# Optimization experiments

Measured on AMD Instinct MI355X. Metric: run time of the kernel, lower is better.

The kernel has to match this reference:

```python
import jax, jax.numpy as jnp
import numpy as np

HID = 4096; H = 32; KVH = 8; D = 128
B = 4; Q = 256; KV = 2048; HIST = KV - Q
BS = 64; NB = KV // BS; NBLOCKS = 160
WINDOW = 1024; THETA = 10000.0


def _rope(x, pos):
    # x: [T, heads, D], pos: [T] absolute positions
    half = D // 2
    inv = 1.0 / (THETA ** (jnp.arange(half, dtype=jnp.float32) / half))
    f = pos.astype(jnp.float32)[:, None] * inv[None, :]          # [T, D/2]
    cos = jnp.concatenate([jnp.cos(f), jnp.cos(f)], -1)[:, None, :]
    sin = jnp.concatenate([jnp.sin(f), jnp.sin(f)], -1)[:, None, :]
    x1, x2 = jnp.split(x, 2, axis=-1)
    return x * cos + jnp.concatenate([-x2, x1], -1) * sin


def setup_inputs() -> dict:
    key = jax.random.key(0)
    ks = jax.random.split(key, 7)
    T = B * Q
    return dict(
        hidden_states=jax.random.normal(ks[0], (T, HID), jnp.float32),
        wq=jax.random.normal(ks[1], (HID, H * D), jnp.float32) * 0.02,
        wk=jax.random.normal(ks[2], (HID, KVH * D), jnp.float32) * 0.02,
        wv=jax.random.normal(ks[3], (HID, KVH * D), jnp.float32) * 0.02,
        wo=jax.random.normal(ks[4], (H * D, HID), jnp.float32) * 0.02,
        k_cache=jax.random.normal(ks[5], (NBLOCKS, BS, KVH, D), jnp.float32),
        v_cache=jax.random.normal(ks[6], (NBLOCKS, BS, KVH, D), jnp.float32),
        # each sequence appends Q new tokens at positions [HIST, KV)
        position_ids=jnp.tile(HIST + jnp.arange(Q, dtype=jnp.int32), B),
        q_start_loc=jnp.arange(B, dtype=jnp.int32) * Q,
        q_seq_length=jnp.full((B,), Q, jnp.int32),
        kv_seq_length=jnp.full((B,), KV, jnp.int32),
        block_offsets=jnp.arange(B * NB, dtype=jnp.int32).reshape(B, NB),
    )


def reference(hidden_states, wq, wk, wv, wo, k_cache, v_cache,
              position_ids, q_start_loc, q_seq_length, kv_seq_length,
              block_offsets):
    # qkv proj (no bias, Mistral)
    q = (hidden_states @ wq).reshape(-1, H, D)    # [T, H, D]
    k = (hidden_states @ wk).reshape(-1, KVH, D)  # [T, KVH, D]
    v = (hidden_states @ wv).reshape(-1, KVH, D)
    # rotary embedding on q, k with per-token absolute positions
    q = _rope(q, position_ids)
    k = _rope(k, position_ids)
    # fill paged KV cache: token with in-sequence slot s of sequence b goes to
    # block block_offsets[b, s // BS], offset s % BS
    b_idx = jnp.repeat(jnp.arange(B), Q)
    blk = block_offsets[b_idx, position_ids // BS]
    off = position_ids % BS
    k_cache = k_cache.at[blk, off].set(k)
    v_cache = v_cache.at[blk, off].set(v)
    # paged attention: gather each sequence's blocks from the cache
    k_all = k_cache[block_offsets].reshape(B, KV, KVH, D)
    v_all = v_cache[block_offsets].reshape(B, KV, KVH, D)
    G = H // KVH  # GQA group size
    qb = q.reshape(B, Q, KVH, G, D)
    scores = jnp.einsum('bqhgd,bkhd->bhgqk', qb, k_all) / jnp.sqrt(jnp.float32(D))
    # causal + sliding-window mask on absolute positions
    qpos = HIST + jnp.arange(Q)
    kpos = jnp.arange(KV)
    valid = (kpos[None, :] <= qpos[:, None]) & (kpos[None, :] > qpos[:, None] - WINDOW)
    scores = jnp.where(valid[None, None, None], scores, -jnp.inf)
    p = jax.nn.softmax(scores, axis=-1)
    o = jnp.einsum('bhgqk,bkhd->bqhgd', p, v_all).reshape(B * Q, H * D)
    return o @ wo
```

## Files before the change

### kernel.cpp

```cpp
#include <hip/hip_runtime.h>

#define BSZ  4
#define QL   256
#define KVL  2048
#define HIST 1792
#define WIN  1024
#define NH   32
#define NKVH 8
#define DH   128
#define HID  4096
#define SCALE 0.088388347648318447f
#define MFIX  8.0f

typedef __bf16 bf16x8 __attribute__((ext_vector_type(8)));
typedef float  fx4    __attribute__((ext_vector_type(4)));
typedef unsigned short us4 __attribute__((ext_vector_type(4)));
typedef unsigned short us8 __attribute__((ext_vector_type(8)));

__device__ __forceinline__ unsigned short f2bf(float x) {
    unsigned u = __float_as_uint(x);
    u += 0x7FFFu + ((u >> 16) & 1u);
    return (unsigned short)(u >> 16);
}
__device__ __forceinline__ float bf2f(unsigned short h) {
    return __uint_as_float(((unsigned)h) << 16);
}
__device__ __forceinline__ fx4 mfma16(bf16x8 a, bf16x8 b, fx4 c) {
    return __builtin_amdgcn_mfma_f32_16x16x32_bf16(a, b, c, 0, 0, 0);
}
__device__ __forceinline__ bf16x8 ldb16(const unsigned short* p) {
    return *reinterpret_cast<const bf16x8*>(p);
}

typedef __attribute__((address_space(1))) const void gv_t;
typedef __attribute__((address_space(3))) void lv_t;
__device__ __forceinline__ void gl16(const void* g, void* l) {
    __builtin_amdgcn_global_load_lds((gv_t*)g, (lv_t*)l, 16, 0, 0);
}

__device__ __forceinline__ void gemm_body(
    const unsigned short* __restrict__ A, const unsigned short* __restrict__ B,
    float* __restrict__ C0, float* __restrict__ Cz, size_t czstride,
    int lda, int ldb, int ldc, int ksteps, int klast, int nx, int ny, int nz)
{
    constexpr int TILE = 128 * 32;
    __shared__ __align__(16) unsigned short lds[3 * 2 * TILE];

    const int per = gridDim.x >> 3;
    const int t = (blockIdx.x & 7) * per + (blockIdx.x >> 3);
    const int bx = t % nx;
    const int by = (t / nx) % ny;
    const int bz = t / (nx * ny);

    const int row0 = bx * 128;
    const int col0 = by * 128;
    const int kbase = bz * ksteps * 32;
    const int nks = (bz == nz - 1) ? klast : ksteps;
    float* Cm = (bz == 0) ? C0 : (Cz + (size_t)(bz - 1) * czstride);

    const int tid  = threadIdx.x;
    const int lane = tid & 63;
    const int w    = tid >> 6;
    const int wr   = w >> 1, wc = w & 1;
    const int l16  = lane & 15;
    const int lg   = lane >> 4;
    const int r_in = lane >> 2;
    const int c8   = (lane & 3) * 8;

    fx4 acc[4][4] = {};

    auto STAGE = [&](int bufi, int kp) {
        unsigned short* Lb = lds + bufi * (2 * TILE);
#pragma unroll
        for (int i = 0; i < 2; ++i) {
            const int r = w * 32 + i * 16 + r_in;
            const int ldsb = (w * 2 + i) * 512;
            gl16(A + (size_t)(row0 + r) * lda + kp + c8, Lb + ldsb);
            gl16(B + (size_t)(col0 + r) * ldb + kp + c8, Lb + TILE + ldsb);
        }
    };

    STAGE(0, kbase);
    STAGE(1, kbase + 32);
    for (int ks = 0; ks < nks; ++ks) {
        if (ks + 2 < nks) {
            STAGE((ks + 2) % 3, kbase + (ks + 2) * 32);
            asm volatile("s_waitcnt vmcnt(8)" ::: "memory");
        } else if (ks + 1 < nks) {
            asm volatile("s_waitcnt vmcnt(4)" ::: "memory");
        } else {
            asm volatile("s_waitcnt vmcnt(0)" ::: "memory");
        }
        __builtin_amdgcn_s_barrier();
        __builtin_amdgcn_sched_barrier(0);

        const unsigned short* Lb = lds + (ks % 3) * (2 * TILE);
        const unsigned short* AhT = Lb;
        const unsigned short* BhT = Lb + TILE;

        bf16x8 af[4], bfv[4];
#pragma unroll
        for (int f = 0; f < 4; ++f) {
            af[f]  = ldb16(AhT + (wr * 64 + f * 16 + l16) * 32 + lg * 8);
            bfv[f] = ldb16(BhT + (wc * 64 + f * 16 + l16) * 32 + lg * 8);
        }
        __builtin_amdgcn_s_setprio(1);
#pragma unroll
        for (int fr = 0; fr < 4; ++fr)
#pragma unroll
            for (int fc = 0; fc < 4; ++fc)
                acc[fr][fc] = mfma16(af[fr], bfv[fc], acc[fr][fc]);
        __builtin_amdgcn_s_setprio(0);
        __builtin_amdgcn_sched_barrier(0);
        __builtin_amdgcn_s_barrier();
    }
#pragma unroll
    for (int fr = 0; fr < 4; ++fr)
#pragma unroll
        for (int fc = 0; fc < 4; ++fc) {
            const size_t rbase = (size_t)(row0 + wr * 64 + fr * 16 + lg * 4);
            const int col = col0 + wc * 64 + fc * 16 + l16;
#pragma unroll
            for (int r = 0; r < 4; ++r)
                Cm[(rbase + r) * ldc + col] = acc[fr][fc][r];
        }
}

__global__ __launch_bounds__(256) void qkv_gemm_kernel(
    const unsigned short* __restrict__ A, const unsigned short* __restrict__ B,
    float* __restrict__ C0, float* __restrict__ Cz, size_t czstride,
    int lda, int ldb, int ldc, int ksteps, int klast, int nx, int ny, int nz)
{
    gemm_body(A, B, C0, Cz, czstride, lda, ldb, ldc, ksteps, klast, nx, ny, nz);
}

__global__ __launch_bounds__(256) void oproj_gemm_kernel(
    const unsigned short* __restrict__ A, const unsigned short* __restrict__ B,
    float* __restrict__ C0, float* __restrict__ Cz, size_t czstride,
    int lda, int ldb, int ldc, int ksteps, int klast, int nx, int ny, int nz)
{
    gemm_body(A, B, C0, Cz, czstride, lda, ldb, ldc, ksteps, klast, nx, ny, nz);
}

__device__ __forceinline__ void transpose_tile(
    const float* __restrict__ w, unsigned short* __restrict__ hi, int N,
    int n0, int k0)
{
    __shared__ unsigned short sh[64][72];
    const int tid = threadIdx.x;
    const int rr = tid >> 4;
    const int cc = (tid & 15) * 4;
#pragma unroll
    for (int p = 0; p < 4; ++p) {
        const int kl = p * 16 + rr;
        fx4 v = *reinterpret_cast<const fx4*>(w + (size_t)(k0 + kl) * N + n0 + cc);
#pragma unroll
        for (int j = 0; j < 4; ++j)
            sh[cc + j][kl] = f2bf(v[j]);
    }
    __syncthreads();
    const int nl = tid >> 2;
    const int kc = (tid & 3) * 16;
    unsigned short* oh = hi + (size_t)(n0 + nl) * 4096 + k0 + kc;
    *reinterpret_cast<us8*>(oh)     = *reinterpret_cast<const us8*>(&sh[nl][kc]);
    *reinterpret_cast<us8*>(oh + 8) = *reinterpret_cast<const us8*>(&sh[nl][kc + 8]);
}

__global__ __launch_bounds__(256) void prep_kernel(
    const float* __restrict__ wq, const float* __restrict__ wk,
    const float* __restrict__ wv, const float* __restrict__ wo,
    const float* __restrict__ hs,
    unsigned short* __restrict__ wqkvT, unsigned short* __restrict__ woTh,
    unsigned short* __restrict__ hsb, float* __restrict__ tab)
{
    const int r = blockIdx.x;
    const int tid = threadIdx.x;
    if (r < 4096) {
        transpose_tile(wq, wqkvT, 4096, (r & 63) * 64, (r >> 6) * 64);
    } else if (r < 5120) {
        const int r2 = r - 4096;
        transpose_tile(wk, wqkvT + (size_t)4096 * 4096, 1024,
                       (r2 & 15) * 64, (r2 >> 4) * 64);
    } else if (r < 6144) {
        const int r2 = r - 5120;
        transpose_tile(wv, wqkvT + (size_t)5120 * 4096, 1024,
                       (r2 & 15) * 64, (r2 >> 4) * 64);
    } else if (r < 10240) {
        const int r2 = r - 6144;
        transpose_tile(wo, woTh, 4096, (r2 & 63) * 64, (r2 >> 6) * 64);
    } else if (r < 12288) {
        const int r2 = r - 10240;
        int i = r2 * 256 + tid;
#pragma unroll
        for (int rep = 0; rep < 2; ++rep) {
            fx4 v = reinterpret_cast<const fx4*>(hs)[i];
            us4 o;
#pragma unroll
            for (int j = 0; j < 4; ++j) o[j] = f2bf(v[j]);
            reinterpret_cast<us4*>(hsb)[i] = o;
            i += 524288;
        }
    } else {
        const int r2 = r - 12288;
        const int qi = r2 * 4 + (tid >> 6);
        const int jr = tid & 63;
        const float inv = powf(10000.f, -(float)jr * (1.f / 64.f));
        const float f = (float)(HIST + qi) * inv;
        float s, c;
        sincosf(f, &s, &c);
        tab[(qi * 64 + jr) * 2]     = c;
        tab[(qi * 64 + jr) * 2 + 1] = s;
    }
}

__global__ __launch_bounds__(256) void rope_q_kernel(
    const float* __restrict__ qkv0, const float* __restrict__ qkv1,
    const int* __restrict__ pos_ids, const float* __restrict__ tab,
    unsigned short* __restrict__ qb)
{
    const int t = blockIdx.x;
    const int b = t >> 8;
    const int qi = t & 255;
    const int pi = pos_ids[t] - HIST;
    const int tid = threadIdx.x;
    const int h = tid >> 3;
    const int d0 = (tid & 7) * 8;
    const float* q0 = qkv0 + (size_t)t * 6144 + h * DH;
    const float* q1 = qkv1 + (size_t)t * 6144 + h * DH;
    float xl[8], xh[8];
    *reinterpret_cast<fx4*>(&xl[0]) = *reinterpret_cast<const fx4*>(q0 + d0)
                                    + *reinterpret_cast<const fx4*>(q1 + d0);
    *reinterpret_cast<fx4*>(&xl[4]) = *reinterpret_cast<const fx4*>(q0 + d0 + 4)
                                    + *reinterpret_cast<const fx4*>(q1 + d0 + 4);
    *reinterpret_cast<fx4*>(&xh[0]) = *reinterpret_cast<const fx4*>(q0 + d0 + 64)
                                    + *reinterpret_cast<const fx4*>(q1 + d0 + 64);
    *reinterpret_cast<fx4*>(&xh[4]) = *reinterpret_cast<const fx4*>(q0 + d0 + 68)
                                    + *reinterpret_cast<const fx4*>(q1 + d0 + 68);
    us8 outl, outh;
#pragma unroll
    for (int i = 0; i < 8; ++i) {
        const int jr = d0 + i;
        const float c = tab[(pi * 64 + jr) * 2];
        const float s = tab[(pi * 64 + jr) * 2 + 1];
        outl[i] = f2bf(xl[i] * c - xh[i] * s);
        outh[i] = f2bf(xh[i] * c + xl[i] * s);
    }
    unsigned short* dst = qb + (((size_t)b * NH + h) * QL + qi) * DH;
    *reinterpret_cast<us8*>(dst + d0)      = outl;
    *reinterpret_cast<us8*>(dst + d0 + 64) = outh;
}

__global__ __launch_bounds__(256) void gather_kv_kernel(
    const float* __restrict__ qkv0, const float* __restrict__ qkv1,
    const float* __restrict__ k_cache, const float* __restrict__ v_cache,
    const int* __restrict__ block_offsets, const float* __restrict__ tab,
    unsigned short* __restrict__ k_all, unsigned short* __restrict__ vT)
{
    __shared__ unsigned short vls[32][136];
    const int bid = blockIdx.x;
    const int xcd = bid & 7;
    const int i = bid >> 3;
    const int g = ((i & 31) << 3) | xcd;
    const int kh = i >> 5;
    const int b  = g >> 6;
    const int ck = g & 63;
    const int kv0 = ck * 32;
    const int tid = threadIdx.x;
    const int tok = tid >> 3;
    const int sl  = tid & 7;
    const int kvpos = kv0 + tok;
    const bool is_old = (kvpos < HIST);

    float x[16];
    float v[16];
    if (is_old) {
        const int blk = block_offsets[b * 32 + (kvpos >> 6)];
        const size_t base = (((size_t)blk * 64 + (kvpos & 63)) * NKVH + kh) * DH + sl * 4;
        const float* sk = k_cache + base;
        const float* sv = v_cache + base;
#pragma unroll
        for (int j = 0; j < 4; ++j) {
            *reinterpret_cast<fx4*>(&x[j * 4]) = *reinterpret_cast<const fx4*>(sk + j * 32);
            *reinterpret_cast<fx4*>(&v[j * 4]) = *reinterpret_cast<const fx4*>(sv + j * 32);
        }
    } else {
        const int t = b * QL + (kvpos - HIST);
        const int pi = kvpos - HIST;
        const size_t tb = (size_t)t * 6144 + kh * DH + sl * 4;
        const float* k0p = qkv0 + tb + 4096;
        const float* k1p = qkv1 + tb + 4096;
        const float* v0p = qkv0 + tb + 5120;
        const float* v1p = qkv1 + tb + 5120;
#pragma unroll
        for (int j = 0; j < 4; ++j) {
            *reinterpret_cast<fx4*>(&x[j * 4]) =
                *reinterpret_cast<const fx4*>(k0p + j * 32) +
                *reinterpret_cast<const fx4*>(k1p + j * 32);
            *reinterpret_cast<fx4*>(&v[j * 4]) =
                *reinterpret_cast<const fx4*>(v0p + j * 32) +
                *reinterpret_cast<const fx4*>(v1p + j * 32);
        }
#pragma unroll
        for (int j = 0; j < 2; ++j) {
            const int jr0 = sl * 4 + j * 32;
            fx4 cs0 = *reinterpret_cast<const fx4*>(tab + ((size_t)pi * 64 + jr0) * 2);
            fx4 cs1 = *reinterpret_cast<const fx4*>(tab + ((size_t)pi * 64 + jr0) * 2 + 4);
            const float c[4] = {cs0[0], cs0[2], cs1[0], cs1[2]};
            const float s[4] = {cs0[1], cs0[3], cs1[1], cs1[3]};
#pragma unroll
            for (int e = 0; e < 4; ++e) {
                const float lo = x[j * 4 + e], hi = x[(j + 2) * 4 + e];
                x[j * 4 + e]       = lo * c[e] - hi * s[e];
                x[(j + 2) * 4 + e] = hi * c[e] + lo * s[e];
            }
        }
    }
    {
        const size_t tbase = (((size_t)b * NKVH + kh) * KVL + kv0) * DH;
#pragma unroll
        for (int j = 0; j < 4; ++j) {
            const int d = sl * 4 + j * 32;
            const int dc = d >> 3;
            us4 pk;
#pragma unroll
            for (int e = 0; e < 4; ++e) pk[e] = f2bf(x[j * 4 + e]);
            *reinterpret_cast<us4*>(k_all + tbase + ((dc * 32 + tok) << 3) + (d & 7)) = pk;
        }
    }
#pragma unroll
    for (int j = 0; j < 4; ++j) {
        us4 pv;
#pragma unroll
        for (int e = 0; e < 4; ++e) pv[e] = f2bf(v[j * 4 + e]);
        *reinterpret_cast<us4*>(&vls[tok][sl * 4 + j * 32]) = pv;
    }
    __syncthreads();
    const int dr = tid >> 1;
    const int half = tid & 1;
    unsigned short* vtile = vT + (((size_t)b * NKVH + kh) * 64 + ck) * 4096;
#pragma unroll
    for (int i2 = 0; i2 < 16; i2 += 8) {
        const int kvc = half * 2 + (i2 >> 3);
        us8 pk;
#pragma unroll
        for (int j = 0; j < 8; ++j) pk[j] = vls[half * 16 + i2 + j][dr];
        *reinterpret_cast<us8*>(vtile + kvc * 1024 + dr * 8) = pk;
    }
}

__global__ __launch_bounds__(512) void attn_kernel(
    const unsigned short* __restrict__ qb,
    const unsigned short* __restrict__ kall,
    const unsigned short* __restrict__ vT,
    unsigned short* __restrict__ ohi)
{
    __shared__ __align__(16) unsigned short ldskv[4 * 8192];
    __shared__ __align__(16) unsigned short plds[8][16][88];

    const int bid = blockIdx.x;
    const int xcd = bid & 7, slot = bid >> 3;
    const int pair = xcd * 4 + (slot >> 3);
    const int within = slot & 7;
    const int kh = pair >> 2, b = pair & 3;
    const int qt = within & 3, p = within >> 2;

    const int tid = threadIdx.x;
    const int lane = tid & 63;
    const int w = tid >> 6;
    const int h = kh * 4 + p * 2 + (w >> 2);
    const int ww = w & 3;
    const int l16 = lane & 15;
    const int lg = lane >> 4;
    const int qrow0 = qt * 64 + ww * 16;
    const int qabs0 = HIST + qrow0;

    const unsigned short* qptr =
        qb + (((size_t)b * NH + h) * QL + qrow0 + l16) * DH + lg * 8;
    bf16x8 qf[4];
#pragma unroll
    for (int ds = 0; ds < 4; ++ds) qf[ds] = ldb16(qptr + ds * 32);

    fx4 oacc[8];
#pragma unroll
    for (int f = 0; f < 8; ++f) oacc[f] = (fx4){0.f, 0.f, 0.f, 0.f};
    float lsum[4] = {0.f, 0.f, 0.f, 0.f};

    const unsigned short* kbase = kall + ((size_t)b * NKVH + kh) * (KVL * DH);
    const unsigned short* vbase = vT + ((size_t)b * NKVH + kh) * (KVL * DH);

    const int kv_lo = ((HIST + qt * 64) - (WIN - 1)) & ~31;

    auto STAGE = [&](int bufi, int kv0) {
        unsigned short* kl = ldskv + bufi * 8192;
        const unsigned short* kg = kbase + (size_t)kv0 * DH;
        const unsigned short* vg = vbase + (size_t)(kv0 >> 5) * 4096;
        const int ci = w * 64 + lane;
        gl16(kg + ci * 8, kl + ci * 8);
        gl16(vg + ci * 8, kl + 4096 + ci * 8);
    };

    auto QK = [&](const unsigned short* kl, fx4& s0, fx4& s1) {
#pragma unroll
        for (int ds = 0; ds < 4; ++ds) {
            bf16x8 kf0 = ldb16(kl + ((ds * 4 + lg) * 32 + l16) * 8);
            bf16x8 kf1 = ldb16(kl + ((ds * 4 + lg) * 32 + 16 + l16) * 8);
            s0 = mfma16(qf[ds], kf0, s0);
            s1 = mfma16(qf[ds], kf1, s1);
        }
    };

    auto SM = [&](int kv0, fx4& s0, fx4& s1, int pc) {
        float p0v[4], p1v[4];
        const bool interior = (kv0 >= qabs0 + 16 - WIN) && (kv0 + 31 <= qabs0);
        if (interior) {
#pragma unroll
            for (int r = 0; r < 4; ++r) {
                p0v[r] = __expf(fmaf(s0[r], SCALE, -MFIX));
                p1v[r] = __expf(fmaf(s1[r], SCALE, -MFIX));
            }
        } else {
            const int kvp0 = kv0 + l16, kvp1 = kvp0 + 16;
#pragma unroll
            for (int r = 0; r < 4; ++r) {
                const int qpos = qabs0 + lg * 4 + r;
                const float e0 = __expf(fmaf(s0[r], SCALE, -MFIX));
                const float e1 = __expf(fmaf(s1[r], SCALE, -MFIX));
                p0v[r] = (kvp0 <= qpos && kvp0 > qpos - WIN) ? e0 : 0.f;
                p1v[r] = (kvp1 <= qpos && kvp1 > qpos - WIN) ? e1 : 0.f;
            }
        }
#pragma unroll
        for (int r = 0; r < 4; ++r) {
            lsum[r] += p0v[r] + p1v[r];
            plds[w][lg * 4 + r][pc + l16] = f2bf(p0v[r]);
            plds[w][lg * 4 + r][pc + 16 + l16] = f2bf(p1v[r]);
        }
    };

    auto PV = [&](const unsigned short* vl, bf16x8 pa) {
#pragma unroll
        for (int f = 0; f < 8; ++f) {
            bf16x8 vf = ldb16(vl + lg * 1024 + (f * 16 + l16) * 8);
            oacc[f] = mfma16(pa, vf, oacc[f]);
        }
    };

    STAGE(0, kv_lo);
    STAGE(1, kv_lo + 32);

    for (int t = 0; t < 34; t += 2) {
        if (t + 2 < 34) {
            STAGE((t + 2) & 3, kv_lo + (t + 2) * 32);
            STAGE((t + 3) & 3, kv_lo + (t + 3) * 32);
            asm volatile("s_waitcnt vmcnt(4)" ::: "memory");
        } else {
            asm volatile("s_waitcnt vmcnt(0)" ::: "memory");
        }
        __builtin_amdgcn_s_barrier();
        __builtin_amdgcn_sched_barrier(0);

        const unsigned short* kl0 = ldskv + (t & 3) * 8192;
        const unsigned short* kl1 = ldskv + ((t + 1) & 3) * 8192;

        fx4 sA0 = (fx4){0.f, 0.f, 0.f, 0.f}, sA1 = (fx4){0.f, 0.f, 0.f, 0.f};
        fx4 sB0 = (fx4){0.f, 0.f, 0.f, 0.f}, sB1 = (fx4){0.f, 0.f, 0.f, 0.f};
        __builtin_amdgcn_s_setprio(1);
        QK(kl0, sA0, sA1);
        QK(kl1, sB0, sB1);
        __builtin_amdgcn_s_setprio(0);

        SM(kv_lo + t * 32, sA0, sA1, 0);
        SM(kv_lo + (t + 1) * 32, sB0, sB1, 40);

        asm volatile("s_waitcnt lgkmcnt(0)" ::: "memory");
        __builtin_amdgcn_sched_barrier(0);
        bf16x8 pa0 = ldb16(&plds[w][l16][0 + lg * 8]);
        bf16x8 pa1 = ldb16(&plds[w][l16][40 + lg * 8]);
        __builtin_amdgcn_s_setprio(1);
        PV(kl0 + 4096, pa0);
        PV(kl1 + 4096, pa1);
        __builtin_amdgcn_s_setprio(0);
        __builtin_amdgcn_sched_barrier(0);
        __builtin_amdgcn_s_barrier();
    }
#pragma unroll
    for (int r = 0; r < 4; ++r) {
#pragma unroll
        for (int off = 1; off < 16; off <<= 1)
            lsum[r] += __shfl_xor(lsum[r], off);
    }
    float rl[4];
#pragma unroll
    for (int r = 0; r < 4; ++r) rl[r] = 1.f / lsum[r];
    const size_t obase = ((size_t)b * QL + qrow0 + lg * 4) * (NH * DH) + h * DH;
#pragma unroll
    for (int f = 0; f < 8; ++f)
#pragma unroll
        for (int r = 0; r < 4; ++r)
            ohi[obase + (size_t)r * (NH * DH) + f * 16 + l16] = f2bf(oacc[f][r] * rl[r]);
}

__global__ __launch_bounds__(256) void reduce_out_kernel(
    float* __restrict__ out, const float* __restrict__ parts)
{
    const int n4 = (1024 * 4096) / 4;
    int i = blockIdx.x * blockDim.x + threadIdx.x;
    for (; i < n4; i += gridDim.x * blockDim.x) {
        fx4 v = reinterpret_cast<fx4*>(out)[i] + reinterpret_cast<const fx4*>(parts)[i];
        reinterpret_cast<fx4*>(out)[i] = v;
    }
}

extern "C" void kernel_launch(void* const* d_in, const int* in_sizes, int n_in,
                              void* d_out, int out_size, void* d_ws, size_t ws_size,
                              hipStream_t stream)
{
    const float* hs = (const float*)d_in[0];
    const float* wq = (const float*)d_in[1];
    const float* wk = (const float*)d_in[2];
    const float* wv = (const float*)d_in[3];
    const float* wo = (const float*)d_in[4];
    const float* kc = (const float*)d_in[5];
    const float* vc = (const float*)d_in[6];
    const int* pos  = (const int*)d_in[7];
    const int* boff = (const int*)d_in[11];
    float* out = (float*)d_out;

    char* ws = (char*)d_ws;
    unsigned short* woTh  = (unsigned short*)(ws + 0);
    unsigned short* wqkvT = (unsigned short*)(ws + 67108864);
    unsigned short* kall  = (unsigned short*)(ws + 67108864);
    unsigned short* vTp   = (unsigned short*)(ws + 83886080);
    unsigned short* ohi   = (unsigned short*)(ws + 100663296);
    float* qkvb           = (float*)(ws + 117440512);
    float* oparts         = (float*)(ws + 117440512);
    unsigned short* hsb   = (unsigned short*)(ws + 167772160);
    unsigned short* qbb   = (unsigned short*)(ws + 167772160);
    float* tab            = (float*)(ws + 176160768);

    prep_kernel<<<12352, 256, 0, stream>>>(wq, wk, wv, wo, hs, wqkvT, woTh, hsb, tab);

    qkv_gemm_kernel<<<768, 256, 0, stream>>>(
        hsb, wqkvT,
        qkvb, qkvb + (size_t)1024 * 6144, (size_t)1024 * 6144,
        4096, 4096, 6144, 64, 64, 8, 48, 2);

    rope_q_kernel<<<1024, 256, 0, stream>>>(qkvb, qkvb + 6291456, pos, tab, qbb);
    gather_kv_kernel<<<2048, 256, 0, stream>>>(qkvb, qkvb + 6291456, kc, vc, boff, tab, kall, vTp);
    attn_kernel<<<256, 512, 0, stream>>>(qbb, kall, vTp, ohi);

    oproj_gemm_kernel<<<512, 256, 0, stream>>>(
        ohi, woTh,
        out, oparts, (size_t)1024 * 4096,
        4096, 4096, 4096, 64, 64, 8, 32, 2);
    reduce_out_kernel<<<2048, 256, 0, stream>>>(out, oparts);
}
```

Before: 231.0 us.

## Switch GEMM to 32x32x16 MFMA with XOR-swizzled LDS layout

Replaces the 4x4 grid of 16x16x32 bf16 MFMAs per wave with a 2x2 grid of 32x32x16 MFMAs, halving fragment loads from LDS per k-step and using the larger instruction. The global-to-LDS staging now XOR-swizzles the 8-element column chunk by row to reduce LDS bank conflicts on the fragment reads. The epilogue is rewritten for the 32x32 accumulator layout. This affects the QKV and output projection GEMMs, and the swizzle and output mapping must match exactly or results break.

```diff
diff --git a/kernel.cpp b/kernel.cpp
--- a/kernel.cpp
+++ b/kernel.cpp
@@ -14,6 +14,7 @@
 
 typedef __bf16 bf16x8 __attribute__((ext_vector_type(8)));
 typedef float  fx4    __attribute__((ext_vector_type(4)));
+typedef float  fx16   __attribute__((ext_vector_type(16)));
 typedef unsigned short us4 __attribute__((ext_vector_type(4)));
 typedef unsigned short us8 __attribute__((ext_vector_type(8)));
 
@@ -27,6 +28,9 @@
 }
 __device__ __forceinline__ fx4 mfma16(bf16x8 a, bf16x8 b, fx4 c) {
     return __builtin_amdgcn_mfma_f32_16x16x32_bf16(a, b, c, 0, 0, 0);
+}
+__device__ __forceinline__ fx16 mfma32(bf16x8 a, bf16x8 b, fx16 c) {
+    return __builtin_amdgcn_mfma_f32_32x32x16_bf16(a, b, c, 0, 0, 0);
 }
 __device__ __forceinline__ bf16x8 ldb16(const unsigned short* p) {
     return *reinterpret_cast<const bf16x8*>(p);
@@ -62,12 +66,11 @@
     const int lane = tid & 63;
     const int w    = tid >> 6;
     const int wr   = w >> 1, wc = w & 1;
-    const int l16  = lane & 15;
-    const int lg   = lane >> 4;
+    const int l32  = lane & 31;
+    const int lk   = lane >> 5;
     const int r_in = lane >> 2;
-    const int c8   = (lane & 3) * 8;
-
-    fx4 acc[4][4] = {};
+
+    fx16 acc[2][2] = {};
 
     auto STAGE = [&](int bufi, int kp) {
         unsigned short* Lb = lds + bufi * (2 * TILE);
@@ -75,6 +78,7 @@
         for (int i = 0; i < 2; ++i) {
             const int r = w * 32 + i * 16 + r_in;
             const int ldsb = (w * 2 + i) * 512;
+            const int c8 = (((lane & 3) ^ (r & 3)) << 3);
             gl16(A + (size_t)(row0 + r) * lda + kp + c8, Lb + ldsb);
             gl16(B + (size_t)(col0 + r) * ldb + kp + c8, Lb + TILE + ldsb);
         }
@@ -98,31 +102,41 @@
         const unsigned short* AhT = Lb;
         const unsigned short* BhT = Lb + TILE;
 
-        bf16x8 af[4], bfv[4];
-#pragma unroll
-        for (int f = 0; f < 4; ++f) {
-            af[f]  = ldb16(AhT + (wr * 64 + f * 16 + l16) * 32 + lg * 8);
-            bfv[f] = ldb16(BhT + (wc * 64 + f * 16 + l16) * 32 + lg * 8);
-        }
+        bf16x8 af[2][2], bfv[2][2];
+#pragma unroll
+        for (int tm = 0; tm < 2; ++tm)
+#pragma unroll
+            for (int kh = 0; kh < 2; ++kh) {
+                const int ra = wr * 64 + tm * 32 + l32;
+                const int ca = ((kh * 2 + lk) ^ (ra & 3)) << 3;
+                af[tm][kh] = ldb16(AhT + ra * 32 + ca);
+                const int rb = wc * 64 + tm * 32 + l32;
+                const int cb = ((kh * 2 + lk) ^ (rb & 3)) << 3;
+                bfv[tm][kh] = ldb16(BhT + rb * 32 + cb);
+            }
         __builtin_amdgcn_s_setprio(1);
 #pragma unroll
-        for (int fr = 0; fr < 4; ++fr)
-#pragma unroll
-            for (int fc = 0; fc < 4; ++fc)
-                acc[fr][fc] = mfma16(af[fr], bfv[fc], acc[fr][fc]);
+        for (int tm = 0; tm < 2; ++tm)
+#pragma unroll
+            for (int tn = 0; tn < 2; ++tn)
+#pragma unroll
+                for (int kh = 0; kh < 2; ++kh)
+                    acc[tm][tn] = mfma32(af[tm][kh], bfv[tn][kh], acc[tm][tn]);
         __builtin_amdgcn_s_setprio(0);
         __builtin_amdgcn_sched_barrier(0);
         __builtin_amdgcn_s_barrier();
     }
 #pragma unroll
-    for (int fr = 0; fr < 4; ++fr)
-#pragma unroll
-        for (int fc = 0; fc < 4; ++fc) {
-            const size_t rbase = (size_t)(row0 + wr * 64 + fr * 16 + lg * 4);
-            const int col = col0 + wc * 64 + fc * 16 + l16;
-#pragma unroll
-            for (int r = 0; r < 4; ++r)
-                Cm[(rbase + r) * ldc + col] = acc[fr][fc][r];
+    for (int tm = 0; tm < 2; ++tm)
+#pragma unroll
+        for (int tn = 0; tn < 2; ++tn) {
+            const size_t rb = (size_t)(row0 + wr * 64 + tm * 32 + 4 * lk);
+            const int cb = col0 + wc * 64 + tn * 32 + l32;
+#pragma unroll
+            for (int reg = 0; reg < 16; ++reg) {
+                const int rr = (reg & 3) + 8 * (reg >> 2);
+                Cm[(rb + rr) * ldc + cb] = acc[tm][tn][reg];
+            }
         }
 }
 
```

After: 242.7 us. 1.05x slower.

## Replace weight transpose with k-grouped bf16 layout read directly by GEMM

Applied to the files above, without the earlier changes.

The prep kernel no longer transposes weights through shared memory. It now writes each weight as bf16 in a [K/8][N][8] packed layout, where each thread reads 8 strided rows and stores a 16-byte vector. The GEMM B-tile staging and fragment loads are rewritten to read this layout, and the QKV kernel picks the q/k/v sub-matrix from the column offset. This removes the LDS transpose cost in prep, but the fp32 reads in prep are now strided per thread and the prep grid roughly doubles.

```diff
diff --git a/kernel.cpp b/kernel.cpp
--- a/kernel.cpp
+++ b/kernel.cpp
@@ -38,16 +38,17 @@
     __builtin_amdgcn_global_load_lds((gv_t*)g, (lv_t*)l, 16, 0, 0);
 }
 
+template<bool QKVB>
 __device__ __forceinline__ void gemm_body(
     const unsigned short* __restrict__ A, const unsigned short* __restrict__ B,
     float* __restrict__ C0, float* __restrict__ Cz, size_t czstride,
-    int lda, int ldb, int ldc, int ksteps, int klast, int nx, int ny, int nz)
+    int lda, int ldc, int ksteps, int klast, int nx, int ny, int nz,
+    int bid, int nblocks, unsigned short* lds)
 {
     constexpr int TILE = 128 * 32;
-    __shared__ __align__(16) unsigned short lds[3 * 2 * TILE];
-
-    const int per = gridDim.x >> 3;
-    const int t = (blockIdx.x & 7) * per + (blockIdx.x >> 3);
+
+    const int per = nblocks >> 3;
+    const int t = (bid & 7) * per + (bid >> 3);
     const int bx = t % nx;
     const int by = (t / nx) % ny;
     const int bz = t / (nx * ny);
@@ -57,6 +58,14 @@
     const int kbase = bz * ksteps * 32;
     const int nks = (bz == nz - 1) ? klast : ksteps;
     float* Cm = (bz == 0) ? C0 : (Cz + (size_t)(bz - 1) * czstride);
+
+    const unsigned short* Bm;
+    int Nw, lc0;
+    if (QKVB) {
+        if (col0 < 4096)      { Bm = B;            Nw = 4096; lc0 = col0; }
+        else if (col0 < 5120) { Bm = B + 16777216; Nw = 1024; lc0 = col0 - 4096; }
+        else                  { Bm = B + 20971520; Nw = 1024; lc0 = col0 - 5120; }
+    } else { Bm = B; Nw = 4096; lc0 = col0; }
 
     const int tid  = threadIdx.x;
     const int lane = tid & 63;
@@ -74,9 +83,13 @@
 #pragma unroll
         for (int i = 0; i < 2; ++i) {
             const int r = w * 32 + i * 16 + r_in;
-            const int ldsb = (w * 2 + i) * 512;
-            gl16(A + (size_t)(row0 + r) * lda + kp + c8, Lb + ldsb);
-            gl16(B + (size_t)(col0 + r) * ldb + kp + c8, Lb + TILE + ldsb);
+            gl16(A + (size_t)(row0 + r) * lda + kp + c8,
+                 Lb + (w * 2 + i) * 512);
+            const int c = i * 256 + tid;
+            const int kg = c >> 7;
+            const int n  = c & 127;
+            gl16(Bm + ((size_t)((kp >> 3) + kg) * Nw + lc0 + n) * 8,
+                 Lb + TILE + (i * 256 + w * 64) * 8);
         }
     };
 
@@ -102,7 +115,7 @@
 #pragma unroll
         for (int f = 0; f < 4; ++f) {
             af[f]  = ldb16(AhT + (wr * 64 + f * 16 + l16) * 32 + lg * 8);
-            bfv[f] = ldb16(BhT + (wc * 64 + f * 16 + l16) * 32 + lg * 8);
+            bfv[f] = ldb16(BhT + (lg * 128 + wc * 64 + f * 16 + l16) * 8);
         }
         __builtin_amdgcn_s_setprio(1);
 #pragma unroll
@@ -128,42 +141,33 @@
 
 __global__ __launch_bounds__(256) void qkv_gemm_kernel(
     const unsigned short* __restrict__ A, const unsigned short* __restrict__ B,
-    float* __restrict__ C0, float* __restrict__ Cz, size_t czstride,
-    int lda, int ldb, int ldc, int ksteps, int klast, int nx, int ny, int nz)
-{
-    gemm_body(A, B, C0, Cz, czstride, lda, ldb, ldc, ksteps, klast, nx, ny, nz);
+    float* __restrict__ C0, float* __restrict__ Cz, size_t czstride)
+{
+    __shared__ __align__(16) unsigned short lds[3 * 2 * 128 * 32];
+    gemm_body<true>(A, B, C0, Cz, czstride, 4096, 6144, 64, 64, 8, 48, 2,
+                    blockIdx.x, 768, lds);
 }
 
 __global__ __launch_bounds__(256) void oproj_gemm_kernel(
     const unsigned short* __restrict__ A, const unsigned short* __restrict__ B,
-    float* __restrict__ C0, float* __restrict__ Cz, size_t czstride,
-    int lda, int ldb, int ldc, int ksteps, int klast, int nx, int ny, int nz)
-{
-    gemm_body(A, B, C0, Cz, czstride, lda, ldb, ldc, ksteps, klast, nx, ny, nz);
-}
-
-__device__ __forceinline__ void transpose_tile(
-    const float* __restrict__ w, unsigned short* __restrict__ hi, int N,
-    int n0, int k0)
-{
-    __shared__ unsigned short sh[64][72];
-    const int tid = threadIdx.x;
-    const int rr = tid >> 4;
-    const int cc = (tid & 15) * 4;
-#pragma unroll
-    for (int p = 0; p < 4; ++p) {
-        const int kl = p * 16 + rr;
-        fx4 v = *reinterpret_cast<const fx4*>(w + (size_t)(k0 + kl) * N + n0 + cc);
-#pragma unroll
-        for (int j = 0; j < 4; ++j)
-            sh[cc + j][kl] = f2bf(v[j]);
-    }
-    __syncthreads();
-    const int nl = tid >> 2;
-    const int kc = (tid & 3) * 16;
-    unsigned short* oh = hi + (size_t)(n0 + nl) * 4096 + k0 + kc;
-    *reinterpret_cast<us8*>(oh)     = *reinterpret_cast<const us8*>(&sh[nl][kc]);
-    *reinterpret_cast<us8*>(oh + 8) = *reinterpret_cast<const us8*>(&sh[nl][kc + 8]);
+    float* __restrict__ C0, float* __restrict__ Cz, size_t czstride)
+{
+    __shared__ __align__(16) unsigned short lds[3 * 2 * 128 * 32];
+    gemm_body<false>(A, B, C0, Cz, czstride, 4096, 4096, 64, 64, 8, 32, 2,
+                     blockIdx.x, 512, lds);
+}
+
+__device__ __forceinline__ void convert_w8(
+    const float* __restrict__ w, unsigned short* __restrict__ out, int N,
+    int kg, int n0)
+{
+    const int n = n0 + threadIdx.x;
+    const float* src = w + (size_t)kg * 8 * N + n;
+    us8 o;
+#pragma unroll
+    for (int j = 0; j < 8; ++j)
+        o[j] = f2bf(src[(size_t)j * N]);
+    *reinterpret_cast<us8*>(out + ((size_t)kg * N + n) * 8) = o;
 }
 
 __global__ __launch_bounds__(256) void prep_kernel(
@@ -175,21 +179,19 @@
 {
     const int r = blockIdx.x;
     const int tid = threadIdx.x;
-    if (r < 4096) {
-        transpose_tile(wq, wqkvT, 4096, (r & 63) * 64, (r >> 6) * 64);
-    } else if (r < 5120) {
-        const int r2 = r - 4096;
-        transpose_tile(wk, wqkvT + (size_t)4096 * 4096, 1024,
-                       (r2 & 15) * 64, (r2 >> 4) * 64);
-    } else if (r < 6144) {
-        const int r2 = r - 5120;
-        transpose_tile(wv, wqkvT + (size_t)5120 * 4096, 1024,
-                       (r2 & 15) * 64, (r2 >> 4) * 64);
+    if (r < 8192) {
+        convert_w8(wq, wqkvT, 4096, r >> 4, (r & 15) * 256);
     } else if (r < 10240) {
-        const int r2 = r - 6144;
-        transpose_tile(wo, woTh, 4096, (r2 & 63) * 64, (r2 >> 6) * 64);
+        const int r2 = r - 8192;
+        convert_w8(wk, wqkvT + 16777216, 1024, r2 >> 2, (r2 & 3) * 256);
     } else if (r < 12288) {
         const int r2 = r - 10240;
+        convert_w8(wv, wqkvT + 20971520, 1024, r2 >> 2, (r2 & 3) * 256);
+    } else if (r < 20480) {
+        const int r2 = r - 12288;
+        convert_w8(wo, woTh, 4096, r2 >> 4, (r2 & 15) * 256);
+    } else if (r < 22528) {
+        const int r2 = r - 20480;
         int i = r2 * 256 + tid;
 #pragma unroll
         for (int rep = 0; rep < 2; ++rep) {
@@ -201,7 +203,7 @@
             i += 524288;
         }
     } else {
-        const int r2 = r - 12288;
+        const int r2 = r - 22528;
         const int qi = r2 * 4 + (tid >> 6);
         const int jr = tid & 63;
         const float inv = powf(10000.f, -(float)jr * (1.f / 64.f));
@@ -538,12 +540,11 @@
     unsigned short* qbb   = (unsigned short*)(ws + 167772160);
     float* tab            = (float*)(ws + 176160768);
 
-    prep_kernel<<<12352, 256, 0, stream>>>(wq, wk, wv, wo, hs, wqkvT, woTh, hsb, tab);
+    prep_kernel<<<22592, 256, 0, stream>>>(wq, wk, wv, wo, hs, wqkvT, woTh, hsb, tab);
 
     qkv_gemm_kernel<<<768, 256, 0, stream>>>(
         hsb, wqkvT,
-        qkvb, qkvb + (size_t)1024 * 6144, (size_t)1024 * 6144,
-        4096, 4096, 6144, 64, 64, 8, 48, 2);
+        qkvb, qkvb + (size_t)1024 * 6144, (size_t)1024 * 6144);
 
     rope_q_kernel<<<1024, 256, 0, stream>>>(qkvb, qkvb + 6291456, pos, tab, qbb);
     gather_kv_kernel<<<2048, 256, 0, stream>>>(qkvb, qkvb + 6291456, kc, vc, boff, tab, kall, vTp);
@@ -551,7 +552,6 @@
 
     oproj_gemm_kernel<<<512, 256, 0, stream>>>(
         ohi, woTh,
-        out, oparts, (size_t)1024 * 4096,
-        4096, 4096, 4096, 64, 64, 8, 32, 2);
+        out, oparts, (size_t)1024 * 4096);
     reduce_out_kernel<<<2048, 256, 0, stream>>>(out, oparts);
 }
```

After: 216.7 us. -6.2%, faster.
